# Optimization experiments

Measured on AMD Instinct MI355X. Metric: run time of the kernel, lower is better.

Reference implementation:

```python
import jax, jax.numpy as jnp
import numpy as np

EMBED_DIM = 512
NUM_HEADS = 8
HEAD_DIM = EMBED_DIM // NUM_HEADS
SCALE = HEAD_DIM ** -0.5
TEMP = 1.0


def setup_inputs() -> dict:
    key = jax.random.key(0)
    ks = jax.random.split(key, 12)
    B, N, Nk, C = 4, 2048, 2048, EMBED_DIM
    s = C ** -0.5
    return {
        "x": jax.random.normal(ks[0], (B, N, C), jnp.float32),
        "y": jax.random.normal(ks[1], (B, Nk, C), jnp.float32),
        "z": jax.random.normal(ks[2], (B, Nk, C), jnp.float32),
        "Wq": jax.random.normal(ks[3], (C, C), jnp.float32) * s,
        "bq": jnp.zeros((C,), jnp.float32),
        "Wk": jax.random.normal(ks[4], (C, C), jnp.float32) * s,
        "bk": jnp.zeros((C,), jnp.float32),
        "Wv": jax.random.normal(ks[5], (C, C), jnp.float32) * s,
        "bv": jnp.zeros((C,), jnp.float32),
        "Wo": jax.random.normal(ks[6], (C, C), jnp.float32) * s,
        "bo": jnp.zeros((C,), jnp.float32),
    }


def reference(x, y, z, Wq, bq, Wk, bk, Wv, bv, Wo, bo):
    B, N, C = x.shape
    Nk = y.shape[1]
    H, D = NUM_HEADS, HEAD_DIM

    def split_heads(t, L):
        return t.reshape(B, L, H, D).transpose(0, 2, 1, 3)  # [B,H,L,D]

    q = split_heads(x @ Wq.T + bq, N)
    k = split_heads(y @ Wk.T + bk, Nk)
    v = split_heads(z @ Wv.T + bv, Nk)

    # [B,H,N,Nk] logits, scaled
    logits = jnp.einsum("bhnd,bhkd->bhnk", q, k) * SCALE

    # Gumbel-softmax (soft, tau=TEMP) with a fixed noise key
    gkey = jax.random.key(42)
    gumbels = jax.random.gumbel(gkey, logits.shape, logits.dtype)
    attn = jax.nn.softmax((logits + gumbels) / TEMP, axis=-1)

    out = jnp.einsum("bhnk,bhkd->bhnd", attn, v)
    out = out.transpose(0, 2, 1, 3).reshape(B, N, C)
    return out @ Wo.T + bo
```

## Files before the change

### kernel.cpp

```cpp
#include <hip/hip_runtime.h>
#include <hip/hip_bf16.h>
#include <stdint.h>

#define Bdim 4
#define Hdim 8
#define Ndim 2048
#define Cdim 512
#define Ddim 64
#define SCALE_F 0.125f
#define SOFTMAX_SHIFT 30.0f
#define KSPLIT 2

typedef __bf16 bf16_t;
typedef __bf16 bf16x8 __attribute__((ext_vector_type(8)));
typedef float f32x4 __attribute__((ext_vector_type(4)));

#define SWZ_XOR_F(v, m) \
  __int_as_float(__builtin_amdgcn_ds_swizzle(__float_as_int(v), (0x1F | ((m) << 10))))

__device__ __forceinline__ float gumbel_noise(uint32_t flat) {
  const uint32_t k0 = 0u, k1 = 42u, k2 = 0x1BD11BDAu ^ 0u ^ 42u;
  uint32_t x0 = 0u;
  uint32_t x1 = flat;
  x0 += k0; x1 += k1;
#define TF_R(r) { x0 += x1; x1 = __builtin_rotateleft32(x1, r); x1 ^= x0; }
#define TF_R4A TF_R(13) TF_R(15) TF_R(26) TF_R(6)
#define TF_R4B TF_R(17) TF_R(29) TF_R(16) TF_R(24)
  TF_R4A  x0 += k1; x1 += k2 + 1u;
  TF_R4B  x0 += k2; x1 += k0 + 2u;
  TF_R4A  x0 += k0; x1 += k1 + 3u;
  TF_R4B  x0 += k1; x1 += k2 + 4u;
  TF_R4A  x0 += k2; x1 += k0 + 5u;
#undef TF_R4B
#undef TF_R4A
#undef TF_R
  uint32_t bits = x0 ^ x1;
  float f = __uint_as_float((bits >> 9) | 0x3F800000u) - 1.0f;
  float u = f + 1.17549435e-38f;
  return -__logf(-__logf(u));
}

__global__ void cvt_f32_bf16(const float* __restrict__ in,
                             bf16_t* __restrict__ out, int n8) {
  int i = blockIdx.x * blockDim.x + threadIdx.x;
  if (i < n8) {
    const float4* p = (const float4*)in + (size_t)i * 2;
    float4 a = p[0], b = p[1];
    union { bf16_t h[8]; uint4 u; } pk;
    pk.h[0] = (bf16_t)a.x; pk.h[1] = (bf16_t)a.y;
    pk.h[2] = (bf16_t)a.z; pk.h[3] = (bf16_t)a.w;
    pk.h[4] = (bf16_t)b.x; pk.h[5] = (bf16_t)b.y;
    pk.h[6] = (bf16_t)b.z; pk.h[7] = (bf16_t)b.w;
    *((uint4*)out + i) = pk.u;
  }
}

__device__ __forceinline__ void gemm_core(const bf16_t* __restrict__ A,
                                          const bf16_t* __restrict__ W,
                                          int m0, int n0,
                                          bf16_t* As, bf16_t* Ws,
                                          f32x4 (&acc)[4][4]) {
  const int t = threadIdx.x;
  const int wave = t >> 6, lane = t & 63;
  const int ln = lane & 15, qd = lane >> 4;
  const int wm = wave >> 1, wn = wave & 1;

#pragma unroll
  for (int i = 0; i < 4; i++)
#pragma unroll
    for (int j = 0; j < 4; j++) acc[i][j] = (f32x4){0.f, 0.f, 0.f, 0.f};

  for (int kt = 0; kt < Cdim / 64; ++kt) {
#pragma unroll
    for (int it = 0; it < 4; ++it) {
      int vec = it * 256 + t;
      int row = vec >> 3, c8 = (vec & 7) * 8;
      *(bf16x8*)&As[row * 72 + c8] =
          *(const bf16x8*)&A[(size_t)(m0 + row) * Cdim + kt * 64 + c8];
      *(bf16x8*)&Ws[row * 72 + c8] =
          *(const bf16x8*)&W[(size_t)(n0 + row) * Cdim + kt * 64 + c8];
    }
    __syncthreads();
#pragma unroll
    for (int ks = 0; ks < 2; ++ks) {
      bf16x8 af[4], bfr[4];
#pragma unroll
      for (int i = 0; i < 4; i++)
        af[i] = *(const bf16x8*)&As[(wm * 64 + i * 16 + ln) * 72 + ks * 32 + qd * 8];
#pragma unroll
      for (int j = 0; j < 4; j++)
        bfr[j] = *(const bf16x8*)&Ws[(wn * 64 + j * 16 + ln) * 72 + ks * 32 + qd * 8];
#pragma unroll
      for (int i = 0; i < 4; i++)
#pragma unroll
        for (int j = 0; j < 4; j++)
          acc[i][j] = __builtin_amdgcn_mfma_f32_16x16x32_bf16(af[i], bfr[j],
                                                              acc[i][j], 0, 0, 0);
    }
    __syncthreads();
  }
}

__global__ __launch_bounds__(256, 2)
void qkv_gemm_kernel(const bf16_t* __restrict__ xb, const bf16_t* __restrict__ yb,
                     const bf16_t* __restrict__ zb, const bf16_t* __restrict__ wqb,
                     const bf16_t* __restrict__ wkb, const bf16_t* __restrict__ wvb,
                     const float* __restrict__ bq, const float* __restrict__ bk,
                     const float* __restrict__ bv, bf16_t* __restrict__ qo,
                     bf16_t* __restrict__ ko, bf16_t* __restrict__ vo) {
  __shared__ bf16_t As[128 * 72];
  __shared__ bf16_t Ws[128 * 72];
  const int sel = blockIdx.z;
  const bf16_t* A = sel == 0 ? xb : (sel == 1 ? yb : zb);
  const bf16_t* W = sel == 0 ? wqb : (sel == 1 ? wkb : wvb);
  const float* bias = sel == 0 ? bq : (sel == 1 ? bk : bv);
  bf16_t* O = sel == 0 ? qo : (sel == 1 ? ko : vo);
  const float mul = sel == 0 ? SCALE_F : 1.0f;
  const int m0 = blockIdx.y * 128, n0 = blockIdx.x * 128;

  f32x4 acc[4][4];
  gemm_core(A, W, m0, n0, As, Ws, acc);

  const int t = threadIdx.x;
  const int wave = t >> 6, lane = t & 63;
  const int ln = lane & 15, qd = lane >> 4;
  const int wm = wave >> 1, wn = wave & 1;
#pragma unroll
  for (int i = 0; i < 4; i++)
#pragma unroll
    for (int j = 0; j < 4; j++)
#pragma unroll
      for (int r = 0; r < 4; r++) {
        int grow = m0 + wm * 64 + i * 16 + qd * 4 + r;
        int gcol = n0 + wn * 64 + j * 16 + ln;
        float val = (acc[i][j][r] + bias[gcol]) * mul;
        int b = grow >> 11, n = grow & 2047;
        int h = gcol >> 6, d = gcol & 63;
        O[(((size_t)b * Hdim + h) * Ndim + n) * Ddim + d] = (bf16_t)val;
      }
}

__global__ __launch_bounds__(256, 2)
void out_gemm_kernel(const bf16_t* __restrict__ ab, const bf16_t* __restrict__ wob,
                     const float* __restrict__ bo, float* __restrict__ out) {
  __shared__ bf16_t As[128 * 72];
  __shared__ bf16_t Ws[128 * 72];
  const int m0 = blockIdx.y * 128, n0 = blockIdx.x * 128;
  f32x4 acc[4][4];
  gemm_core(ab, wob, m0, n0, As, Ws, acc);

  const int t = threadIdx.x;
  const int wave = t >> 6, lane = t & 63;
  const int ln = lane & 15, qd = lane >> 4;
  const int wm = wave >> 1, wn = wave & 1;
#pragma unroll
  for (int i = 0; i < 4; i++)
#pragma unroll
    for (int j = 0; j < 4; j++)
#pragma unroll
      for (int r = 0; r < 4; r++) {
        int grow = m0 + wm * 64 + i * 16 + qd * 4 + r;
        int gcol = n0 + wn * 64 + j * 16 + ln;
        out[(size_t)grow * Cdim + gcol] = acc[i][j][r] + bo[gcol];
      }
}

__global__ __launch_bounds__(256, 4)
void attn_kernel(const bf16_t* __restrict__ qb, const bf16_t* __restrict__ kb,
                 const bf16_t* __restrict__ vb, float* __restrict__ part_o,
                 float* __restrict__ part_l) {
  __shared__ bf16_t Ks[64 * 72];
  __shared__ bf16_t Vt[64 * 72];
  __shared__ bf16_t Ps[64 * 72];

  const int t = threadIdx.x;
  const int wave = t >> 6, lane = t & 63;
  const int ln = lane & 15, qd = lane >> 4;
  const int qtile = blockIdx.x;
  const int bh = blockIdx.y;
  const int z = blockIdx.z;
  const int qbase = qtile * 64;
  const int kt_lo = z * (Ndim / 64 / KSPLIT);
  const int kt_hi = kt_lo + (Ndim / 64 / KSPLIT);

  const bf16_t* Qg = qb + (size_t)bh * Ndim * Ddim;
  const bf16_t* Kg = kb + (size_t)bh * Ndim * Ddim;
  const bf16_t* Vg = vb + (size_t)bh * Ndim * Ddim;

  const bf16_t* Qrow = Qg + (size_t)(qbase + wave * 16 + ln) * Ddim;
  bf16x8 qf0 = *(const bf16x8*)&Qrow[qd * 8];
  bf16x8 qf1 = *(const bf16x8*)&Qrow[32 + qd * 8];

  float l_r[4] = {0.f, 0.f, 0.f, 0.f};
  f32x4 o_acc[4];
#pragma unroll
  for (int j = 0; j < 4; j++) o_acc[j] = (f32x4){0.f, 0.f, 0.f, 0.f};

  const uint32_t flat_bh = (uint32_t)bh << 22;

  for (int kt = kt_lo; kt < kt_hi; ++kt) {
#pragma unroll
    for (int it = 0; it < 2; ++it) {
      int vec = it * 256 + t;
      int row = vec >> 3, c8 = (vec & 7) * 8;
      *(bf16x8*)&Ks[row * 72 + c8] =
          *(const bf16x8*)&Kg[(size_t)(kt * 64 + row) * Ddim + c8];
      bf16x8 vv = *(const bf16x8*)&Vg[(size_t)(kt * 64 + row) * Ddim + c8];
      int swz_base = ((row >> 3) ^ (c8 >> 3)) * 8 + (row & 7);
#pragma unroll
      for (int jj = 0; jj < 8; jj++)
        Vt[(c8 + jj) * 72 + swz_base] = vv[jj];
    }
    __syncthreads();

    f32x4 s[4];
#pragma unroll
    for (int j = 0; j < 4; j++) s[j] = (f32x4){0.f, 0.f, 0.f, 0.f};
#pragma unroll
    for (int j = 0; j < 4; j++) {
      bf16x8 bk0 = *(const bf16x8*)&Ks[(j * 16 + ln) * 72 + qd * 8];
      bf16x8 bk1 = *(const bf16x8*)&Ks[(j * 16 + ln) * 72 + 32 + qd * 8];
      s[j] = __builtin_amdgcn_mfma_f32_16x16x32_bf16(qf0, bk0, s[j], 0, 0, 0);
      s[j] = __builtin_amdgcn_mfma_f32_16x16x32_bf16(qf1, bk1, s[j], 0, 0, 0);
    }

#pragma unroll
    for (int r = 0; r < 4; r++) {
      int qrow = qbase + wave * 16 + qd * 4 + r;
      uint32_t fbase = flat_bh + ((uint32_t)qrow << 11) + (uint32_t)(kt * 64 + ln);
#pragma unroll
      for (int j = 0; j < 4; j++) {
        float sv = s[j][r] + gumbel_noise(fbase + j * 16) - SOFTMAX_SHIFT;
        float pv = __expf(sv);
        l_r[r] += pv;
        Ps[(wave * 16 + qd * 4 + r) * 72 + j * 16 + ln] = (bf16_t)pv;
      }
    }

#pragma unroll
    for (int ks = 0; ks < 2; ++ks) {
      bf16x8 af = *(const bf16x8*)&Ps[(wave * 16 + ln) * 72 + ks * 32 + qd * 8];
#pragma unroll
      for (int j = 0; j < 4; j++) {
        int d = j * 16 + ln;
        bf16x8 bv8 = *(const bf16x8*)&Vt[d * 72 + (((ks * 4 + qd) ^ (d >> 3)) << 3)];
        o_acc[j] = __builtin_amdgcn_mfma_f32_16x16x32_bf16(af, bv8, o_acc[j], 0, 0, 0);
      }
    }
    __syncthreads();
  }

  const int pidx = ((bh << 5) | qtile) * KSPLIT + z;
  float* po = part_o + (size_t)pidx * 64 * 64;
  float* pl = part_l + (size_t)pidx * 64;

#pragma unroll
  for (int r = 0; r < 4; r++) {
    float lsum = l_r[r];
    lsum += SWZ_XOR_F(lsum, 1);
    lsum += SWZ_XOR_F(lsum, 2);
    lsum += SWZ_XOR_F(lsum, 4);
    lsum += SWZ_XOR_F(lsum, 8);
    if (ln == 0) pl[wave * 16 + qd * 4 + r] = lsum;
  }
#pragma unroll
  for (int j = 0; j < 4; j++)
#pragma unroll
    for (int r = 0; r < 4; r++) {
      int row = wave * 16 + qd * 4 + r;
      int col = j * 16 + ln;
      po[row * 64 + col] = o_acc[j][r];
    }
}

__global__ __launch_bounds__(256, 8)
void attn_combine(const float* __restrict__ part_o,
                  const float* __restrict__ part_l, bf16_t* __restrict__ ab) {
  const int blk = blockIdx.x;
  const int bh = blk >> 5, qtile = blk & 31;
  const float* o0 = part_o + (size_t)(blk * KSPLIT + 0) * 64 * 64;
  const float* o1 = part_o + (size_t)(blk * KSPLIT + 1) * 64 * 64;
  const float* l0 = part_l + (size_t)(blk * KSPLIT + 0) * 64;
  const float* l1 = part_l + (size_t)(blk * KSPLIT + 1) * 64;

  const int t = threadIdx.x;
  const int row = t >> 2, c0 = (t & 3) * 16;
  const float linv = 1.0f / (l0[row] + l1[row]);
  const int b = bh >> 3, h = bh & 7;
  bf16_t* dst = ab + ((size_t)b * Ndim + qtile * 64 + row) * Cdim + h * 64 + c0;

#pragma unroll
  for (int i = 0; i < 4; i++) {
    float4 a = *(const float4*)&o0[row * 64 + c0 + i * 4];
    float4 c = *(const float4*)&o1[row * 64 + c0 + i * 4];
    union { bf16_t h4[4]; uint2 u; } pk;
    pk.h4[0] = (bf16_t)((a.x + c.x) * linv);
    pk.h4[1] = (bf16_t)((a.y + c.y) * linv);
    pk.h4[2] = (bf16_t)((a.z + c.z) * linv);
    pk.h4[3] = (bf16_t)((a.w + c.w) * linv);
    *(uint2*)&dst[i * 4] = pk.u;
  }
}

extern "C" void kernel_launch(void* const* d_in, const int* in_sizes, int n_in,
                              void* d_out, int out_size, void* d_ws, size_t ws_size,
                              hipStream_t stream) {
  const float* x  = (const float*)d_in[0];
  const float* y  = (const float*)d_in[1];
  const float* z  = (const float*)d_in[2];
  const float* Wq = (const float*)d_in[3];
  const float* bq = (const float*)d_in[4];
  const float* Wk = (const float*)d_in[5];
  const float* bk = (const float*)d_in[6];
  const float* Wv = (const float*)d_in[7];
  const float* bv = (const float*)d_in[8];
  const float* Wo = (const float*)d_in[9];
  const float* bo = (const float*)d_in[10];
  float* out = (float*)d_out;

  bf16_t* base = (bf16_t*)d_ws;
  const size_t NBIG = (size_t)Bdim * Ndim * Cdim;
  const size_t NW   = (size_t)Cdim * Cdim;
  bf16_t* xb  = base;
  bf16_t* yb  = xb + NBIG;
  bf16_t* zb  = yb + NBIG;
  bf16_t* wqb = zb + NBIG;
  bf16_t* wkb = wqb + NW;
  bf16_t* wvb = wkb + NW;
  bf16_t* wob = wvb + NW;
  bf16_t* qb  = wob + NW;
  bf16_t* kb  = qb + NBIG;
  bf16_t* vb  = kb + NBIG;
  bf16_t* ab  = vb + NBIG;
  float* part_o = (float*)(ab + NBIG);
  float* part_l = part_o + (size_t)1024 * KSPLIT * 64 * 64;

  int n8b = (int)(NBIG / 8), n8w = (int)(NW / 8);
  cvt_f32_bf16<<<n8b / 256, 256, 0, stream>>>(x, xb, n8b);
  cvt_f32_bf16<<<n8b / 256, 256, 0, stream>>>(y, yb, n8b);
  cvt_f32_bf16<<<n8b / 256, 256, 0, stream>>>(z, zb, n8b);
  cvt_f32_bf16<<<n8w / 256, 256, 0, stream>>>(Wq, wqb, n8w);
  cvt_f32_bf16<<<n8w / 256, 256, 0, stream>>>(Wk, wkb, n8w);
  cvt_f32_bf16<<<n8w / 256, 256, 0, stream>>>(Wv, wvb, n8w);
  cvt_f32_bf16<<<n8w / 256, 256, 0, stream>>>(Wo, wob, n8w);

  qkv_gemm_kernel<<<dim3(Cdim / 128, (Bdim * Ndim) / 128, 3), 256, 0, stream>>>(
      xb, yb, zb, wqb, wkb, wvb, bq, bk, bv, qb, kb, vb);

  attn_kernel<<<dim3(Ndim / 64, Bdim * Hdim, KSPLIT), 256, 0, stream>>>(
      qb, kb, vb, part_o, part_l);

  attn_combine<<<dim3(1024), 256, 0, stream>>>(part_o, part_l, ab);

  out_gemm_kernel<<<dim3(Cdim / 128, (Bdim * Ndim) / 128), 256, 0, stream>>>(
      ab, wob, bo, out);
}
```

Baseline: 494.2 us.

## Fold Gumbel noise into a multiplicative factor, prefetch K/V, split keys four ways

Computes exp(s+g) as exp2(s*log2e) * (-1/log u), so each element needs one fewer log and drops the fixed softmax shift. K/V tiles for the next step are now prefetched into registers while the current tile is being computed. KSPLIT rises from 2 to 4 to put more blocks on the GPU. Partial outputs are stored in bf16 and the combine kernel is generalized to sum any number of splits. Without the shift, values rely on float range, and bf16 partials lower precision.

```diff
diff --git a/kernel.cpp b/kernel.cpp
--- a/kernel.cpp
+++ b/kernel.cpp
@@ -8,8 +8,8 @@
 #define Cdim 512
 #define Ddim 64
 #define SCALE_F 0.125f
-#define SOFTMAX_SHIFT 30.0f
-#define KSPLIT 2
+#define KSPLIT 4
+#define LOG2E 1.44269504f
 
 typedef __bf16 bf16_t;
 typedef __bf16 bf16x8 __attribute__((ext_vector_type(8)));
@@ -18,7 +18,7 @@
 #define SWZ_XOR_F(v, m) \
   __int_as_float(__builtin_amdgcn_ds_swizzle(__float_as_int(v), (0x1F | ((m) << 10))))
 
-__device__ __forceinline__ float gumbel_noise(uint32_t flat) {
+__device__ __forceinline__ float gumbel_pfac(uint32_t flat) {
   const uint32_t k0 = 0u, k1 = 42u, k2 = 0x1BD11BDAu ^ 0u ^ 42u;
   uint32_t x0 = 0u;
   uint32_t x1 = flat;
@@ -37,7 +37,7 @@
   uint32_t bits = x0 ^ x1;
   float f = __uint_as_float((bits >> 9) | 0x3F800000u) - 1.0f;
   float u = f + 1.17549435e-38f;
-  return -__logf(-__logf(u));
+  return -__builtin_amdgcn_rcpf(__builtin_amdgcn_logf(u));
 }
 
 __global__ void cvt_f32_bf16(const float* __restrict__ in,
@@ -167,7 +167,7 @@
 
 __global__ __launch_bounds__(256, 4)
 void attn_kernel(const bf16_t* __restrict__ qb, const bf16_t* __restrict__ kb,
-                 const bf16_t* __restrict__ vb, float* __restrict__ part_o,
+                 const bf16_t* __restrict__ vb, bf16_t* __restrict__ part_o,
                  float* __restrict__ part_l) {
   __shared__ bf16_t Ks[64 * 72];
   __shared__ bf16_t Vt[64 * 72];
@@ -191,6 +191,16 @@
   bf16x8 qf0 = *(const bf16x8*)&Qrow[qd * 8];
   bf16x8 qf1 = *(const bf16x8*)&Qrow[32 + qd * 8];
 
+  const int row0 = t >> 3,        c80 = (t & 7) * 8;
+  const int row1 = (256 + t) >> 3, c81 = ((256 + t) & 7) * 8;
+  const int swz0 = ((row0 >> 3) ^ (c80 >> 3)) * 8 + (row0 & 7);
+  const int swz1 = ((row1 >> 3) ^ (c81 >> 3)) * 8 + (row1 & 7);
+
+  bf16x8 kr0 = *(const bf16x8*)&Kg[(size_t)(kt_lo * 64 + row0) * Ddim + c80];
+  bf16x8 kr1 = *(const bf16x8*)&Kg[(size_t)(kt_lo * 64 + row1) * Ddim + c81];
+  bf16x8 vr0 = *(const bf16x8*)&Vg[(size_t)(kt_lo * 64 + row0) * Ddim + c80];
+  bf16x8 vr1 = *(const bf16x8*)&Vg[(size_t)(kt_lo * 64 + row1) * Ddim + c81];
+
   float l_r[4] = {0.f, 0.f, 0.f, 0.f};
   f32x4 o_acc[4];
 #pragma unroll
@@ -199,19 +209,20 @@
   const uint32_t flat_bh = (uint32_t)bh << 22;
 
   for (int kt = kt_lo; kt < kt_hi; ++kt) {
-#pragma unroll
-    for (int it = 0; it < 2; ++it) {
-      int vec = it * 256 + t;
-      int row = vec >> 3, c8 = (vec & 7) * 8;
-      *(bf16x8*)&Ks[row * 72 + c8] =
-          *(const bf16x8*)&Kg[(size_t)(kt * 64 + row) * Ddim + c8];
-      bf16x8 vv = *(const bf16x8*)&Vg[(size_t)(kt * 64 + row) * Ddim + c8];
-      int swz_base = ((row >> 3) ^ (c8 >> 3)) * 8 + (row & 7);
-#pragma unroll
-      for (int jj = 0; jj < 8; jj++)
-        Vt[(c8 + jj) * 72 + swz_base] = vv[jj];
-    }
+    *(bf16x8*)&Ks[row0 * 72 + c80] = kr0;
+    *(bf16x8*)&Ks[row1 * 72 + c81] = kr1;
+#pragma unroll
+    for (int jj = 0; jj < 8; jj++) Vt[(c80 + jj) * 72 + swz0] = vr0[jj];
+#pragma unroll
+    for (int jj = 0; jj < 8; jj++) Vt[(c81 + jj) * 72 + swz1] = vr1[jj];
     __syncthreads();
+
+    if (kt + 1 < kt_hi) {
+      kr0 = *(const bf16x8*)&Kg[(size_t)((kt + 1) * 64 + row0) * Ddim + c80];
+      kr1 = *(const bf16x8*)&Kg[(size_t)((kt + 1) * 64 + row1) * Ddim + c81];
+      vr0 = *(const bf16x8*)&Vg[(size_t)((kt + 1) * 64 + row0) * Ddim + c80];
+      vr1 = *(const bf16x8*)&Vg[(size_t)((kt + 1) * 64 + row1) * Ddim + c81];
+    }
 
     f32x4 s[4];
 #pragma unroll
@@ -230,8 +241,8 @@
       uint32_t fbase = flat_bh + ((uint32_t)qrow << 11) + (uint32_t)(kt * 64 + ln);
 #pragma unroll
       for (int j = 0; j < 4; j++) {
-        float sv = s[j][r] + gumbel_noise(fbase + j * 16) - SOFTMAX_SHIFT;
-        float pv = __expf(sv);
+        float pf = gumbel_pfac(fbase + j * 16);
+        float pv = __builtin_amdgcn_exp2f(s[j][r] * LOG2E) * pf;
         l_r[r] += pv;
         Ps[(wave * 16 + qd * 4 + r) * 72 + j * 16 + ln] = (bf16_t)pv;
       }
@@ -251,7 +262,7 @@
   }
 
   const int pidx = ((bh << 5) | qtile) * KSPLIT + z;
-  float* po = part_o + (size_t)pidx * 64 * 64;
+  bf16_t* po = part_o + (size_t)pidx * 64 * 64;
   float* pl = part_l + (size_t)pidx * 64;
 
 #pragma unroll
@@ -269,37 +280,47 @@
     for (int r = 0; r < 4; r++) {
       int row = wave * 16 + qd * 4 + r;
       int col = j * 16 + ln;
-      po[row * 64 + col] = o_acc[j][r];
+      po[row * 64 + col] = (bf16_t)o_acc[j][r];
     }
 }
 
 __global__ __launch_bounds__(256, 8)
-void attn_combine(const float* __restrict__ part_o,
+void attn_combine(const bf16_t* __restrict__ part_o,
                   const float* __restrict__ part_l, bf16_t* __restrict__ ab) {
   const int blk = blockIdx.x;
   const int bh = blk >> 5, qtile = blk & 31;
-  const float* o0 = part_o + (size_t)(blk * KSPLIT + 0) * 64 * 64;
-  const float* o1 = part_o + (size_t)(blk * KSPLIT + 1) * 64 * 64;
-  const float* l0 = part_l + (size_t)(blk * KSPLIT + 0) * 64;
-  const float* l1 = part_l + (size_t)(blk * KSPLIT + 1) * 64;
-
   const int t = threadIdx.x;
   const int row = t >> 2, c0 = (t & 3) * 16;
-  const float linv = 1.0f / (l0[row] + l1[row]);
+
+  float l = 0.f;
+#pragma unroll
+  for (int zz = 0; zz < KSPLIT; zz++)
+    l += part_l[(size_t)(blk * KSPLIT + zz) * 64 + row];
+  const float linv = 1.0f / l;
+
+  float acc[16];
+#pragma unroll
+  for (int i = 0; i < 16; i++) acc[i] = 0.f;
+#pragma unroll
+  for (int zz = 0; zz < KSPLIT; zz++) {
+    const bf16_t* po =
+        part_o + (size_t)(blk * KSPLIT + zz) * 64 * 64 + row * 64 + c0;
+    bf16x8 a0 = *(const bf16x8*)&po[0];
+    bf16x8 a1 = *(const bf16x8*)&po[8];
+#pragma unroll
+    for (int i = 0; i < 8; i++) { acc[i] += (float)a0[i]; acc[8 + i] += (float)a1[i]; }
+  }
+
   const int b = bh >> 3, h = bh & 7;
   bf16_t* dst = ab + ((size_t)b * Ndim + qtile * 64 + row) * Cdim + h * 64 + c0;
-
-#pragma unroll
-  for (int i = 0; i < 4; i++) {
-    float4 a = *(const float4*)&o0[row * 64 + c0 + i * 4];
-    float4 c = *(const float4*)&o1[row * 64 + c0 + i * 4];
-    union { bf16_t h4[4]; uint2 u; } pk;
-    pk.h4[0] = (bf16_t)((a.x + c.x) * linv);
-    pk.h4[1] = (bf16_t)((a.y + c.y) * linv);
-    pk.h4[2] = (bf16_t)((a.z + c.z) * linv);
-    pk.h4[3] = (bf16_t)((a.w + c.w) * linv);
-    *(uint2*)&dst[i * 4] = pk.u;
-  }
+  union { bf16_t h8[8]; uint4 u; } pk0, pk1;
+#pragma unroll
+  for (int i = 0; i < 8; i++) {
+    pk0.h8[i] = (bf16_t)(acc[i] * linv);
+    pk1.h8[i] = (bf16_t)(acc[8 + i] * linv);
+  }
+  *(uint4*)&dst[0] = pk0.u;
+  *(uint4*)&dst[8] = pk1.u;
 }
 
 extern "C" void kernel_launch(void* const* d_in, const int* in_sizes, int n_in,
@@ -332,8 +353,8 @@
   bf16_t* kb  = qb + NBIG;
   bf16_t* vb  = kb + NBIG;
   bf16_t* ab  = vb + NBIG;
-  float* part_o = (float*)(ab + NBIG);
-  float* part_l = part_o + (size_t)1024 * KSPLIT * 64 * 64;
+  bf16_t* part_o = ab + NBIG;
+  float* part_l = (float*)(part_o + (size_t)1024 * KSPLIT * 64 * 64);
 
   int n8b = (int)(NBIG / 8), n8w = (int)(NW / 8);
   cvt_f32_bf16<<<n8b / 256, 256, 0, stream>>>(x, xb, n8b);
```

After: 440.5 us. -10.9%, faster.
